# Kernel tuning notes

Hardware: AMD Instinct MI355X
Metric: run time of the kernel (lower is better)

The kernel has to match this reference:

```python
import jax, jax.numpy as jnp
import numpy as np


def setup_inputs() -> dict:
    key = jax.random.key(0)
    k1, k2, k3 = jax.random.split(key, 3)
    B, C, H, W = 4, 16, 64, 64
    F, K = 32, 3
    x = jax.random.normal(k1, (B, C, H, W), dtype=jnp.float32)
    # Pade coefficients per (out_channel, in_channel, a, b): numerator deg 5, denom deg 4.
    nums = jax.random.normal(k2, (F, C, K, K, 6), dtype=jnp.float32) * 0.3
    denoms = jax.random.normal(k3, (F, C, K, K, 4), dtype=jnp.float32) * 0.3
    return {"x": x, "nums": nums, "denoms": denoms}


def _rational_conv(x, nums, denoms):
    B, C, H, W = x.shape
    F, _, K, _, _ = nums.shape
    p = (K - 1) // 2
    # pad spatially, move channels last: (B, H+2p, W+2p, C)
    xp = jnp.pad(x, ((0, 0), (0, 0), (p, p), (p, p))).transpose(0, 2, 3, 1)
    # im2col patches: stack the K*K shifted views -> (B, H, W, K2, C)
    patches = jnp.stack(
        [xp[:, a:a + H, b:b + W, :] for a in range(K) for b in range(K)], axis=3
    )
    # powers x^0..x^5 built by repeated multiply (safe for negative bases)
    pws = [jnp.ones_like(patches)]
    for _ in range(5):
        pws.append(pws[-1] * patches)
    pw = jnp.stack(pws, axis=-1)                         # (B,H,W,K2,C,6)
    nums_r = nums.reshape(F, C, K * K, 6)                # (a,b) flattened a*K+b, matches patch order
    denoms_r = denoms.reshape(F, C, K * K, 4)
    # P(x) = sum_n a_n x^n ; Q(x) = 1 + |sum_m b_m x^m|, m=1..4  (Pade version A)
    P = jnp.einsum('bhwkcn,fckn->bhwfkc', pw, nums_r)
    Q = 1.0 + jnp.abs(jnp.einsum('bhwkcm,fckm->bhwfkc', pw[..., 1:5], denoms_r))
    out = (P / Q).sum(axis=(4, 5))                       # (B,H,W,F)
    return out.transpose(0, 3, 1, 2)                     # (B,F,H,W)


def reference(x, nums, denoms):
    return _rational_conv(x, nums, denoms)
```

## Files before the change

### kernel.cpp

```cpp
#include <hip/hip_runtime.h>
#include <hip/hip_fp16.h>

#define B_ 4
#define C_ 16
#define H_ 64
#define W_ 64
#define F_ 32
#define S_ 66
#define CHW_ (S_ * S_)
#define XN_ (B_ * 8 * CHW_)
#define CPAIR 90
#define CN_ (F_ * 8 * CPAIR)

typedef _Float16 hvec2 __attribute__((ext_vector_type(2)));

__global__ __launch_bounds__(256)
void pack_x_kernel(const float* __restrict__ x, __half2* __restrict__ xw) {
    const int i = blockIdx.x * 256 + threadIdx.x;
    if (i >= XN_) return;
    const int cc = i % S_;
    int t = i / S_;
    const int r  = t % S_;
    t /= S_;
    const int pr = t % 8;
    const int b  = t / 8;
    float lo = 0.f, hi = 0.f;
    if (r >= 1 && r <= H_ && cc >= 1 && cc <= W_) {
        const int sp = (r - 1) * W_ + (cc - 1);
        lo = x[((size_t)(b * C_ + pr)     ) * (H_ * W_) + sp];
        hi = x[((size_t)(b * C_ + pr + 8)) * (H_ * W_) + sp];
    }
    xw[i] = __halves2half2(__float2half_rn(lo), __float2half_rn(hi));
}

__global__ __launch_bounds__(256)
void pack_coef_kernel(const float* __restrict__ nums, const float* __restrict__ denoms,
                      __half2* __restrict__ cw) {
    const int i = blockIdx.x * 256 + threadIdx.x;
    if (i >= F_ * 8 * 9) return;
    const int tap = i % 9;
    const int pr  = (i / 9) % 8;
    const int f   = i / 72;
    __half2* o = cw + ((size_t)(f * 8 + pr) * 9 + tap) * 10;
    const size_t nlo = (((size_t)f * C_ + pr)     * 9 + tap) * 6;
    const size_t nhi = (((size_t)f * C_ + pr + 8) * 9 + tap) * 6;
    for (int k = 0; k < 6; ++k)
        o[k] = __halves2half2(__float2half_rn(nums[nlo + k]), __float2half_rn(nums[nhi + k]));
    const size_t dlo = (((size_t)f * C_ + pr)     * 9 + tap) * 4;
    const size_t dhi = (((size_t)f * C_ + pr + 8) * 9 + tap) * 4;
    for (int k = 0; k < 4; ++k)
        o[6 + k] = __halves2half2(__float2half_rn(denoms[dlo + k]), __float2half_rn(denoms[dhi + k]));
}

__global__ __launch_bounds__(256)
void ka_rconv_kernel(const __half2* __restrict__ xw,
                     const __half2* __restrict__ cw,
                     float* __restrict__ out) {
    __shared__ float red[3 * 4 * 64];

    const int tid = threadIdx.x;
    const int col = tid & 63;
    const int wg  = tid >> 6;

    int bid = blockIdx.x;
    const int f  = bid & 31;  bid >>= 5;
    const int t4 = bid & 15;  bid >>= 4;
    const int b  = bid;
    const int gy0 = t4 * 4;

    const __half2 one = __halves2half2(__half(1.0f), __half(1.0f));
    float acc[4] = {0.f, 0.f, 0.f, 0.f};

    for (int cp = 0; cp < 2; ++cp) {
        const int pr = __builtin_amdgcn_readfirstlane(wg * 2 + cp);
        const __half2* xbase = xw + ((size_t)(b * 8 + pr) * S_ + gy0) * S_ + col;
        const __half2* ce = cw + (size_t)(f * 8 + pr) * CPAIR;

        uint3 rv[6];
        #pragma unroll
        for (int k = 0; k < 6; ++k)
            rv[k] = *(const uint3*)(xbase + k * S_);

        #pragma unroll
        for (int t = 0; t < 9; ++t) {
            const __half2 n0 = ce[t*10+0], n1 = ce[t*10+1], n2 = ce[t*10+2];
            const __half2 n3 = ce[t*10+3], n4 = ce[t*10+4], n5 = ce[t*10+5];
            const __half2 d0 = ce[t*10+6], d1 = ce[t*10+7];
            const __half2 d2 = ce[t*10+8], d3 = ce[t*10+9];
            const int a = t / 3, j = t % 3;
            #pragma unroll
            for (int p = 0; p < 4; ++p) {
                const uint3 r3 = rv[p + a];
                const unsigned u = (j == 0) ? r3.x : (j == 1) ? r3.y : r3.z;
                const __half2 xp = __builtin_bit_cast(__half2, u);

                __half2 P = __hfma2(n5, xp, n4);
                P = __hfma2(P, xp, n3);
                P = __hfma2(P, xp, n2);
                P = __hfma2(P, xp, n1);
                P = __hfma2(P, xp, n0);

                __half2 Sd = __hfma2(d3, xp, d2);
                Sd = __hfma2(Sd, xp, d1);
                Sd = __hfma2(Sd, xp, d0);
                Sd = __hmul2(Sd, xp);

                const __half2 Q = __hadd2(one, __habs2(Sd));
                const __half2 R = h2rcp(Q);
                acc[p] = __builtin_amdgcn_fdot2(__builtin_bit_cast(hvec2, P),
                                                __builtin_bit_cast(hvec2, R),
                                                acc[p], false);
            }
        }
    }

    if (wg > 0) {
        #pragma unroll
        for (int p = 0; p < 4; ++p)
            red[((wg - 1) * 4 + p) * 64 + col] = acc[p];
    }
    __syncthreads();
    if (wg == 0) {
        float* op = out + (((size_t)b * F_ + f) * H_ + gy0) * W_ + col;
        #pragma unroll
        for (int p = 0; p < 4; ++p) {
            float s = acc[p] + red[(0 * 4 + p) * 64 + col]
                             + red[(1 * 4 + p) * 64 + col]
                             + red[(2 * 4 + p) * 64 + col];
            op[p * W_] = s;
        }
    }
}

extern "C" void kernel_launch(void* const* d_in, const int* in_sizes, int n_in,
                              void* d_out, int out_size, void* d_ws, size_t ws_size,
                              hipStream_t stream) {
    const float* x      = (const float*)d_in[0];
    const float* nums   = (const float*)d_in[1];
    const float* denoms = (const float*)d_in[2];
    float* outp = (float*)d_out;
    __half2* xw = (__half2*)d_ws;
    __half2* cwp = xw + XN_;

    pack_x_kernel<<<(XN_ + 255) / 256, 256, 0, stream>>>(x, xw);
    pack_coef_kernel<<<(F_ * 8 * 9 + 255) / 256, 256, 0, stream>>>(nums, denoms, cwp);
    dim3 grid(B_ * 16 * F_);
    ka_rconv_kernel<<<grid, 256, 0, stream>>>(xw, cwp, outp);
}
```

Before: 79.83 us.

## Merge pack kernels and give each wave one channel pair over 8 rows

```diff
diff --git a/kernel.cpp b/kernel.cpp
--- a/kernel.cpp
+++ b/kernel.cpp
@@ -10,53 +10,51 @@
 #define CHW_ (S_ * S_)
 #define XN_ (B_ * 8 * CHW_)
 #define CPAIR 90
-#define CN_ (F_ * 8 * CPAIR)
+#define NC_ (F_ * 8 * 9)
 
 typedef _Float16 hvec2 __attribute__((ext_vector_type(2)));
 
 __global__ __launch_bounds__(256)
-void pack_x_kernel(const float* __restrict__ x, __half2* __restrict__ xw) {
+void pack_kernel(const float* __restrict__ x,
+                 const float* __restrict__ nums, const float* __restrict__ denoms,
+                 __half2* __restrict__ xw, __half2* __restrict__ cw) {
     const int i = blockIdx.x * 256 + threadIdx.x;
-    if (i >= XN_) return;
-    const int cc = i % S_;
-    int t = i / S_;
-    const int r  = t % S_;
-    t /= S_;
-    const int pr = t % 8;
-    const int b  = t / 8;
-    float lo = 0.f, hi = 0.f;
-    if (r >= 1 && r <= H_ && cc >= 1 && cc <= W_) {
-        const int sp = (r - 1) * W_ + (cc - 1);
-        lo = x[((size_t)(b * C_ + pr)     ) * (H_ * W_) + sp];
-        hi = x[((size_t)(b * C_ + pr + 8)) * (H_ * W_) + sp];
+    if (i < XN_) {
+        const int cc = i % S_;
+        int t = i / S_;
+        const int r  = t % S_;
+        t /= S_;
+        const int pr = t % 8;
+        const int b  = t / 8;
+        float lo = 0.f, hi = 0.f;
+        if (r >= 1 && r <= H_ && cc >= 1 && cc <= W_) {
+            const int sp = (r - 1) * W_ + (cc - 1);
+            lo = x[((size_t)(b * C_ + pr)     ) * (H_ * W_) + sp];
+            hi = x[((size_t)(b * C_ + pr + 8)) * (H_ * W_) + sp];
+        }
+        xw[i] = __halves2half2(__float2half_rn(lo), __float2half_rn(hi));
+    } else if (i < XN_ + NC_) {
+        const int k = i - XN_;
+        const int tap = k % 9;
+        const int pr  = (k / 9) % 8;
+        const int f   = k / 72;
+        __half2* o = cw + ((size_t)(f * 8 + pr) * 9 + tap) * 10;
+        const size_t nlo = (((size_t)f * C_ + pr)     * 9 + tap) * 6;
+        const size_t nhi = (((size_t)f * C_ + pr + 8) * 9 + tap) * 6;
+        for (int q = 0; q < 6; ++q)
+            o[q] = __halves2half2(__float2half_rn(nums[nlo + q]), __float2half_rn(nums[nhi + q]));
+        const size_t dlo = (((size_t)f * C_ + pr)     * 9 + tap) * 4;
+        const size_t dhi = (((size_t)f * C_ + pr + 8) * 9 + tap) * 4;
+        for (int q = 0; q < 4; ++q)
+            o[6 + q] = __halves2half2(__float2half_rn(denoms[dlo + q]), __float2half_rn(denoms[dhi + q]));
     }
-    xw[i] = __halves2half2(__float2half_rn(lo), __float2half_rn(hi));
 }
 
-__global__ __launch_bounds__(256)
-void pack_coef_kernel(const float* __restrict__ nums, const float* __restrict__ denoms,
-                      __half2* __restrict__ cw) {
-    const int i = blockIdx.x * 256 + threadIdx.x;
-    if (i >= F_ * 8 * 9) return;
-    const int tap = i % 9;
-    const int pr  = (i / 9) % 8;
-    const int f   = i / 72;
-    __half2* o = cw + ((size_t)(f * 8 + pr) * 9 + tap) * 10;
-    const size_t nlo = (((size_t)f * C_ + pr)     * 9 + tap) * 6;
-    const size_t nhi = (((size_t)f * C_ + pr + 8) * 9 + tap) * 6;
-    for (int k = 0; k < 6; ++k)
-        o[k] = __halves2half2(__float2half_rn(nums[nlo + k]), __float2half_rn(nums[nhi + k]));
-    const size_t dlo = (((size_t)f * C_ + pr)     * 9 + tap) * 4;
-    const size_t dhi = (((size_t)f * C_ + pr + 8) * 9 + tap) * 4;
-    for (int k = 0; k < 4; ++k)
-        o[6 + k] = __halves2half2(__float2half_rn(denoms[dlo + k]), __float2half_rn(denoms[dhi + k]));
-}
-
-__global__ __launch_bounds__(256)
+__global__ __launch_bounds__(512)
 void ka_rconv_kernel(const __half2* __restrict__ xw,
                      const __half2* __restrict__ cw,
                      float* __restrict__ out) {
-    __shared__ float red[3 * 4 * 64];
+    __shared__ float red[7 * 8 * 64];
 
     const int tid = threadIdx.x;
     const int col = tid & 63;
@@ -64,69 +62,68 @@
 
     int bid = blockIdx.x;
     const int f  = bid & 31;  bid >>= 5;
-    const int t4 = bid & 15;  bid >>= 4;
+    const int t8 = bid & 7;   bid >>= 3;
     const int b  = bid;
-    const int gy0 = t4 * 4;
+    const int gy0 = t8 * 8;
+
+    const int pr = __builtin_amdgcn_readfirstlane(wg);
+    const __half2* ce = cw + (size_t)(f * 8 + pr) * CPAIR;
+    const __half2* xbase = xw + ((size_t)(b * 8 + pr) * S_ + gy0) * S_ + col;
 
     const __half2 one = __halves2half2(__half(1.0f), __half(1.0f));
-    float acc[4] = {0.f, 0.f, 0.f, 0.f};
+    float acc[8] = {0.f, 0.f, 0.f, 0.f, 0.f, 0.f, 0.f, 0.f};
 
-    for (int cp = 0; cp < 2; ++cp) {
-        const int pr = __builtin_amdgcn_readfirstlane(wg * 2 + cp);
-        const __half2* xbase = xw + ((size_t)(b * 8 + pr) * S_ + gy0) * S_ + col;
-        const __half2* ce = cw + (size_t)(f * 8 + pr) * CPAIR;
+    uint3 rv[10];
+    #pragma unroll
+    for (int k = 0; k < 10; ++k)
+        rv[k] = *(const uint3*)(xbase + k * S_);
 
-        uint3 rv[6];
+    #pragma unroll
+    for (int t = 0; t < 9; ++t) {
+        const __half2 n0 = ce[t*10+0], n1 = ce[t*10+1], n2 = ce[t*10+2];
+        const __half2 n3 = ce[t*10+3], n4 = ce[t*10+4], n5 = ce[t*10+5];
+        const __half2 d0 = ce[t*10+6], d1 = ce[t*10+7];
+        const __half2 d2 = ce[t*10+8], d3 = ce[t*10+9];
+        const int a = t / 3, j = t % 3;
         #pragma unroll
-        for (int k = 0; k < 6; ++k)
-            rv[k] = *(const uint3*)(xbase + k * S_);
+        for (int p = 0; p < 8; ++p) {
+            const uint3 r3 = rv[p + a];
+            const unsigned u = (j == 0) ? r3.x : (j == 1) ? r3.y : r3.z;
+            const __half2 xp = __builtin_bit_cast(__half2, u);
 
-        #pragma unroll
-        for (int t = 0; t < 9; ++t) {
-            const __half2 n0 = ce[t*10+0], n1 = ce[t*10+1], n2 = ce[t*10+2];
-            const __half2 n3 = ce[t*10+3], n4 = ce[t*10+4], n5 = ce[t*10+5];
-            const __half2 d0 = ce[t*10+6], d1 = ce[t*10+7];
-            const __half2 d2 = ce[t*10+8], d3 = ce[t*10+9];
-            const int a = t / 3, j = t % 3;
-            #pragma unroll
-            for (int p = 0; p < 4; ++p) {
-                const uint3 r3 = rv[p + a];
-                const unsigned u = (j == 0) ? r3.x : (j == 1) ? r3.y : r3.z;
-                const __half2 xp = __builtin_bit_cast(__half2, u);
+            __half2 P = __hfma2(n5, xp, n4);
+            P = __hfma2(P, xp, n3);
+            P = __hfma2(P, xp, n2);
+            P = __hfma2(P, xp, n1);
+            P = __hfma2(P, xp, n0);
 
-                __half2 P = __hfma2(n5, xp, n4);
-                P = __hfma2(P, xp, n3);
-                P = __hfma2(P, xp, n2);
-                P = __hfma2(P, xp, n1);
-                P = __hfma2(P, xp, n0);
+            __half2 Sd = __hfma2(d3, xp, d2);
+            Sd = __hfma2(Sd, xp, d1);
+            Sd = __hfma2(Sd, xp, d0);
+            Sd = __hmul2(Sd, xp);
 
-                __half2 Sd = __hfma2(d3, xp, d2);
-                Sd = __hfma2(Sd, xp, d1);
-                Sd = __hfma2(Sd, xp, d0);
-                Sd = __hmul2(Sd, xp);
-
-                const __half2 Q = __hadd2(one, __habs2(Sd));
-                const __half2 R = h2rcp(Q);
-                acc[p] = __builtin_amdgcn_fdot2(__builtin_bit_cast(hvec2, P),
-                                                __builtin_bit_cast(hvec2, R),
-                                                acc[p], false);
-            }
+            const __half2 Q = __hadd2(one, __habs2(Sd));
+            const __half2 R = h2rcp(Q);
+            acc[p] = __builtin_amdgcn_fdot2(__builtin_bit_cast(hvec2, P),
+                                            __builtin_bit_cast(hvec2, R),
+                                            acc[p], false);
         }
     }
 
     if (wg > 0) {
         #pragma unroll
-        for (int p = 0; p < 4; ++p)
-            red[((wg - 1) * 4 + p) * 64 + col] = acc[p];
+        for (int p = 0; p < 8; ++p)
+            red[((wg - 1) * 8 + p) * 64 + col] = acc[p];
     }
     __syncthreads();
     if (wg == 0) {
         float* op = out + (((size_t)b * F_ + f) * H_ + gy0) * W_ + col;
         #pragma unroll
-        for (int p = 0; p < 4; ++p) {
-            float s = acc[p] + red[(0 * 4 + p) * 64 + col]
-                             + red[(1 * 4 + p) * 64 + col]
-                             + red[(2 * 4 + p) * 64 + col];
+        for (int p = 0; p < 8; ++p) {
+            float s = acc[p];
+            #pragma unroll
+            for (int q = 0; q < 7; ++q)
+                s += red[(q * 8 + p) * 64 + col];
             op[p * W_] = s;
         }
     }
@@ -142,8 +139,7 @@
     __half2* xw = (__half2*)d_ws;
     __half2* cwp = xw + XN_;
 
-    pack_x_kernel<<<(XN_ + 255) / 256, 256, 0, stream>>>(x, xw);
-    pack_coef_kernel<<<(F_ * 8 * 9 + 255) / 256, 256, 0, stream>>>(nums, denoms, cwp);
-    dim3 grid(B_ * 16 * F_);
-    ka_rconv_kernel<<<grid, 256, 0, stream>>>(xw, cwp, outp);
+    pack_kernel<<<(XN_ + NC_ + 255) / 256, 256, 0, stream>>>(x, nums, denoms, xw, cwp);
+    dim3 grid(B_ * 8 * F_);
+    ka_rconv_kernel<<<grid, 512, 0, stream>>>(xw, cwp, outp);
 }
```

After: 78.64 us. Within noise of the previous version (-1.5%).
